# Kernel tuning notes

Hardware: AMD Instinct MI355X
Metric: run time of the kernel (lower is better)

Reference implementation:

```python
import jax, jax.numpy as jnp
import numpy as np

K = 3            # kernel size (odd)
CO, CI = 16, 16  # out/in channels

def setup_inputs() -> dict:
    key = jax.random.key(0)
    k1, k2, k3, k4 = jax.random.split(key, 4)
    B, C, H, W = 4, CI, 128, 128
    input_data = jax.random.normal(k1, (B, C, H, W), dtype=jnp.float32)
    # fixation coordinates in pixel units
    foa_xy = jax.random.uniform(k2, (B, 2), dtype=jnp.float32) * jnp.array([W, H], jnp.float32)
    hidden = 256
    W1 = jax.random.normal(k3, (2, hidden), dtype=jnp.float32) * (1.0 / jnp.sqrt(2.0))
    b1 = jnp.zeros((hidden,), jnp.float32)
    W2 = jax.random.normal(k4, (hidden, CO * CI * K * K), dtype=jnp.float32) * (1.0 / jnp.sqrt(hidden))
    b2 = jnp.zeros((CO * CI * K * K,), jnp.float32)
    return {"input_data": input_data, "foa_xy": foa_xy, "W1": W1, "b1": b1, "W2": W2, "b2": b2}

def _unfold_reflect(x, k):
    # x: [B, C, H, W] -> patches [B, C, k*k, H*W], reflect padding, stride 1, dilation 1
    B, C, H, W = x.shape
    pad = (k - 1) // 2
    xp = jnp.pad(x, ((0, 0), (0, 0), (pad, pad), (pad, pad)), mode="reflect")
    rows = [xp[:, :, i:i + H, j:j + W] for i in range(k) for j in range(k)]
    return jnp.stack(rows, axis=2).reshape(B, C, k * k, H * W)

def reference(input_data, foa_xy, W1, b1, W2, b2):
    B, C, H, W = input_data.shape
    # coordinate grid [H*W, 2] as (x, y), matching torch meshgrid(ij) + stack(xx, yy)
    ys = jnp.arange(H, dtype=jnp.float32)
    xs = jnp.arange(W, dtype=jnp.float32)
    yy, xx = jnp.meshgrid(ys, xs, indexing="ij")
    coords = jnp.stack([xx.ravel(), yy.ravel()], axis=1)         # [HW, 2]
    net_in = (coords[None, :, :] - foa_xy[:, None, :]).reshape(B * H * W, 2)
    # kernel-generating MLP
    h = jax.nn.relu(net_in @ W1 + b1)
    net_out = h @ W2 + b2                                        # [B*HW, CO*CI*K*K]
    kernel = net_out.reshape(B, H * W, CO, CI, K * K)            # [B, P, o, i, q]
    patches = _unfold_reflect(input_data, K)                     # [B, CI, K*K, HW]
    # per-pixel conv: sum over in-channels and kernel taps
    out = jnp.einsum("biqp,bpoiq->bop", patches, kernel)         # [B, CO, HW]
    return out.reshape(B, CO, H, W)
```

## Files before the change

kernel.cpp:

```cpp
#include <hip/hip_runtime.h>

#define CI    16
#define CO    16
#define HID   256
#define KPAD  288
#define NKK   9
#define NCH   144
#define IMGH  128
#define IMGW  128
#define PTS   66
#define KKSTR (NCH * 32)
#define OSTRS (NKK * NCH * 32)

typedef float f32x4  __attribute__((ext_vector_type(4)));
typedef float f32x2  __attribute__((ext_vector_type(2)));
typedef short bf16x8 __attribute__((ext_vector_type(8)));

__device__ __host__ __forceinline__ short f2bf(float f) {
  union { float f; unsigned u; } c; c.f = f;
  unsigned b = c.u + 0x7FFFu + ((c.u >> 16) & 1u);
  return (short)(b >> 16);
}

__global__ void prep_w2(const float* __restrict__ W2, const float* __restrict__ b2,
                        short* __restrict__ W2b) {
  __shared__ float tile[32][65];
  const int kk = blockIdx.x % NKK;
  const int colbase = (blockIdx.x / NKK) * 64;
  const int tid = threadIdx.x;

  for (int e = tid; e < 2048; e += 256) {
    int klr = e >> 6;
    int cc  = e & 63;
    int col = colbase + cc;
    float v;
    if (kk < 8) v = W2[(kk * 32 + klr) * (CO * NCH) + col];
    else        v = (klr == 0) ? b2[col] : 0.f;
    tile[klr][cc] = v;
  }
  __syncthreads();
  for (int e = tid; e < 2048; e += 256) {
    int cc = e >> 5;
    int kl = e & 31;
    int col = colbase + cc;
    int o = col / NCH;
    int n = col - o * NCH;
    W2b[(((o * NKK + kk) * NCH + n) << 5) + kl] = f2bf(tile[kl][cc]);
  }
}

__global__ __launch_bounds__(256, 2)
void ngconv_main(const float* __restrict__ in, const float* __restrict__ foa,
                 const float* __restrict__ W1, const float* __restrict__ b1,
                 const short* __restrict__ W2b, float* __restrict__ out) {
  __shared__ short shHf[36 * 512];
  __shared__ float shPatchT[NCH * PTS];

  const int tid  = threadIdx.x;
  const int lane = tid & 63;
  const int wv   = tid >> 6;
  const int c15  = lane & 15;
  const int quad = lane >> 4;

  const int blk = blockIdx.x;
  const int b   = blk >> 8;
  const int rem = blk & 255;
  const int y   = rem >> 1;
  const int x0  = (rem & 1) << 6;

  const float fx  = foa[b * 2 + 0];
  const float fy  = foa[b * 2 + 1];
  const float dyv = (float)y - fy;

  const int ry0 = (y == 0) ? 1 : (y - 1);
  const int ry2 = (y == IMGH - 1) ? (IMGH - 2) : (y + 1);

  for (int e = tid; e < NCH * 64; e += 256) {
    int n  = e >> 6;
    int px = e & 63;
    int i = n / 9, q = n - i * 9;
    int dyr = q / 3, dx = q - dyr * 3;
    int ryr = (dyr == 0) ? ry0 : ((dyr == 1) ? y : ry2);
    int x = x0 + px + dx - 1;
    x = (x < 0) ? 1 : ((x > IMGW - 1) ? (IMGW - 2) : x);
    shPatchT[n * PTS + px] = in[((b * CI + i) * IMGH + ryr) * IMGW + x];
  }

  for (int g = tid; g < 64 * 36; g += 256) {
    int px = g & 63;
    int ks = g >> 6;
    int k0 = ks << 3;
    float dxv = (float)(x0 + px) - fx;
    short hv[8];
    if (k0 < HID) {
      #pragma unroll
      for (int j = 0; j < 8; ++j) {
        int k = k0 + j;
        float h = fmaxf(fmaf(dxv, W1[k], fmaf(dyv, W1[HID + k], b1[k])), 0.f);
        hv[j] = f2bf(h);
      }
    } else {
      #pragma unroll
      for (int j = 0; j < 8; ++j) hv[j] = (k0 + j == HID) ? f2bf(1.f) : (short)0;
    }
    int ms = px >> 4;
    int kk = k0 >> 5;
    int lslot = ((k0 & 31) >> 3) * 16 + (px & 15);
    *(bf16x8*)&shHf[((ms * NKK + kk) << 9) + (lslot << 3)] = *(bf16x8*)hv;
  }
  __syncthreads();

  #pragma unroll 1
  for (int oj = 0; oj < 4; ++oj) {
    const int o = wv + oj * 4;
    const short* Bo = W2b + o * OSTRS + (c15 << 5) + (quad << 3);

    f32x2 P2[8];
    #pragma unroll
    for (int t = 0; t < 8; ++t) P2[t] = (f32x2){0.f, 0.f};

    #pragma unroll 1
    for (int pass = 0; pass < 3; ++pass) {
      const short* Bp = Bo + (pass * 3) * 512;
      f32x4 acc[4][3];
      #pragma unroll
      for (int ms = 0; ms < 4; ++ms)
        #pragma unroll
        for (int j = 0; j < 3; ++j)
          acc[ms][j] = (f32x4){0.f, 0.f, 0.f, 0.f};

      bf16x8 bE[3], bO[3];
      #pragma unroll
      for (int j = 0; j < 3; ++j) bE[j] = *(const bf16x8*)&Bp[j << 9];

      #pragma unroll 1
      for (int t = 0; t < 4; ++t) {
        const int kkE = 2 * t;
        #pragma unroll
        for (int j = 0; j < 3; ++j)
          bO[j] = *(const bf16x8*)&Bp[(kkE + 1) * KKSTR + (j << 9)];
        {
          const short* hp = shHf + (kkE << 9) + (lane << 3);
          #pragma unroll
          for (int ms = 0; ms < 4; ++ms) {
            bf16x8 af = *(const bf16x8*)&hp[ms * (NKK << 9)];
            #pragma unroll
            for (int j = 0; j < 3; ++j)
              acc[ms][j] = __builtin_amdgcn_mfma_f32_16x16x32_bf16(
                  af, bE[j], acc[ms][j], 0, 0, 0);
          }
        }
        #pragma unroll
        for (int j = 0; j < 3; ++j)
          bE[j] = *(const bf16x8*)&Bp[(kkE + 2) * KKSTR + (j << 9)];
        {
          const short* hp = shHf + ((kkE + 1) << 9) + (lane << 3);
          #pragma unroll
          for (int ms = 0; ms < 4; ++ms) {
            bf16x8 af = *(const bf16x8*)&hp[ms * (NKK << 9)];
            #pragma unroll
            for (int j = 0; j < 3; ++j)
              acc[ms][j] = __builtin_amdgcn_mfma_f32_16x16x32_bf16(
                  af, bO[j], acc[ms][j], 0, 0, 0);
          }
        }
      }
      {
        const short* hp = shHf + (8 << 9) + (lane << 3);
        #pragma unroll
        for (int ms = 0; ms < 4; ++ms) {
          bf16x8 af = *(const bf16x8*)&hp[ms * (NKK << 9)];
          #pragma unroll
          for (int j = 0; j < 3; ++j)
            acc[ms][j] = __builtin_amdgcn_mfma_f32_16x16x32_bf16(
                af, bE[j], acc[ms][j], 0, 0, 0);
        }
      }

      #pragma unroll
      for (int j = 0; j < 3; ++j) {
        int n15 = ((pass * 3 + j) << 4) + c15;
        const float* prow = &shPatchT[n15 * PTS + (quad << 2)];
        #pragma unroll
        for (int ms = 0; ms < 4; ++ms) {
          f32x2 p01 = *(const f32x2*)&prow[ms * 16];
          f32x2 p23 = *(const f32x2*)&prow[ms * 16 + 2];
          f32x2 a01 = {acc[ms][j][0], acc[ms][j][1]};
          f32x2 a23 = {acc[ms][j][2], acc[ms][j][3]};
          P2[ms * 2 + 0] += a01 * p01;
          P2[ms * 2 + 1] += a23 * p23;
        }
      }
    }

    float P[16];
    #pragma unroll
    for (int t = 0; t < 16; ++t) P[t] = P2[t >> 1][t & 1];
    #pragma unroll
    for (int m = 8; m >= 1; m >>= 1) {
      const bool hi = (c15 & m) != 0;
      #pragma unroll
      for (int j = 0; j < m; ++j) {
        float keep = hi ? P[j + m] : P[j];
        float send = hi ? P[j] : P[j + m];
        float recv = __shfl_xor(send, m, 64);
        P[j] = keep + recv;
      }
    }

    const int x = x0 + (c15 >> 2) * 16 + quad * 4 + (c15 & 3);
    out[((b * CO + o) * IMGH + y) * IMGW + x] = P[0];
  }
}

extern "C" void kernel_launch(void* const* d_in, const int* in_sizes, int n_in,
                              void* d_out, int out_size, void* d_ws, size_t ws_size,
                              hipStream_t stream) {
  const float* in  = (const float*)d_in[0];
  const float* foa = (const float*)d_in[1];
  const float* W1  = (const float*)d_in[2];
  const float* b1  = (const float*)d_in[3];
  const float* W2  = (const float*)d_in[4];
  const float* b2  = (const float*)d_in[5];
  float* out = (float*)d_out;
  short* W2b = (short*)d_ws;

  prep_w2<<<324, 256, 0, stream>>>(W2, b2, W2b);
  ngconv_main<<<1024, 256, 0, stream>>>(in, foa, W1, b1, W2b, out);
}
```

Before: 190.0 us.

## Shrink LDS footprint with bf16 patches and register bias fragment to raise occupancy

Patch values are now stored in LDS as bf16 instead of fp32, with the row pitch changed to 68, and unpacked with shifts at use. The bias block of the hidden matrix is no longer kept in LDS; a constant register fragment with a 1.0 in the first element of quad 0 supplies it to the ninth MFMA k-step. Together these cut shared memory per block, and launch bounds now request 3 blocks per CU so more waves can hide latency. The trade-offs are lower precision for the input patches and tighter register limits under the new occupancy target.

Result: faster. 182.9 us (-3.8%).

```diff
diff --git a/kernel.cpp b/kernel.cpp
--- a/kernel.cpp
+++ b/kernel.cpp
@@ -5,10 +5,11 @@
 #define HID   256
 #define KPAD  288
 #define NKK   9
+#define NKH   8
 #define NCH   144
 #define IMGH  128
 #define IMGW  128
-#define PTS   66
+#define PTS   68
 #define KKSTR (NCH * 32)
 #define OSTRS (NKK * NCH * 32)
 
@@ -49,12 +50,12 @@
   }
 }
 
-__global__ __launch_bounds__(256, 2)
+__global__ __launch_bounds__(256, 3)
 void ngconv_main(const float* __restrict__ in, const float* __restrict__ foa,
                  const float* __restrict__ W1, const float* __restrict__ b1,
                  const short* __restrict__ W2b, float* __restrict__ out) {
-  __shared__ short shHf[36 * 512];
-  __shared__ float shPatchT[NCH * PTS];
+  __shared__ short shHf[32 * 512];
+  __shared__ short shPatchT[NCH * PTS];
 
   const int tid  = threadIdx.x;
   const int lane = tid & 63;
@@ -83,31 +84,30 @@
     int ryr = (dyr == 0) ? ry0 : ((dyr == 1) ? y : ry2);
     int x = x0 + px + dx - 1;
     x = (x < 0) ? 1 : ((x > IMGW - 1) ? (IMGW - 2) : x);
-    shPatchT[n * PTS + px] = in[((b * CI + i) * IMGH + ryr) * IMGW + x];
-  }
-
-  for (int g = tid; g < 64 * 36; g += 256) {
+    shPatchT[n * PTS + px] = f2bf(in[((b * CI + i) * IMGH + ryr) * IMGW + x]);
+  }
+
+  for (int g = tid; g < 64 * 32; g += 256) {
     int px = g & 63;
     int ks = g >> 6;
     int k0 = ks << 3;
     float dxv = (float)(x0 + px) - fx;
     short hv[8];
-    if (k0 < HID) {
-      #pragma unroll
-      for (int j = 0; j < 8; ++j) {
-        int k = k0 + j;
-        float h = fmaxf(fmaf(dxv, W1[k], fmaf(dyv, W1[HID + k], b1[k])), 0.f);
-        hv[j] = f2bf(h);
-      }
-    } else {
-      #pragma unroll
-      for (int j = 0; j < 8; ++j) hv[j] = (k0 + j == HID) ? f2bf(1.f) : (short)0;
+    #pragma unroll
+    for (int j = 0; j < 8; ++j) {
+      int k = k0 + j;
+      float h = fmaxf(fmaf(dxv, W1[k], fmaf(dyv, W1[HID + k], b1[k])), 0.f);
+      hv[j] = f2bf(h);
     }
     int ms = px >> 4;
     int kk = k0 >> 5;
     int lslot = ((k0 & 31) >> 3) * 16 + (px & 15);
-    *(bf16x8*)&shHf[((ms * NKK + kk) << 9) + (lslot << 3)] = *(bf16x8*)hv;
-  }
+    *(bf16x8*)&shHf[((ms * NKH + kk) << 9) + (lslot << 3)] = *(bf16x8*)hv;
+  }
+
+  bf16x8 af8 = (bf16x8){0, 0, 0, 0, 0, 0, 0, 0};
+  if (quad == 0) af8[0] = (short)0x3F80;
+
   __syncthreads();
 
   #pragma unroll 1
@@ -143,7 +143,7 @@
           const short* hp = shHf + (kkE << 9) + (lane << 3);
           #pragma unroll
           for (int ms = 0; ms < 4; ++ms) {
-            bf16x8 af = *(const bf16x8*)&hp[ms * (NKK << 9)];
+            bf16x8 af = *(const bf16x8*)&hp[ms * (NKH << 9)];
             #pragma unroll
             for (int j = 0; j < 3; ++j)
               acc[ms][j] = __builtin_amdgcn_mfma_f32_16x16x32_bf16(
@@ -157,7 +157,7 @@
           const short* hp = shHf + ((kkE + 1) << 9) + (lane << 3);
           #pragma unroll
           for (int ms = 0; ms < 4; ++ms) {
-            bf16x8 af = *(const bf16x8*)&hp[ms * (NKK << 9)];
+            bf16x8 af = *(const bf16x8*)&hp[ms * (NKH << 9)];
             #pragma unroll
             for (int j = 0; j < 3; ++j)
               acc[ms][j] = __builtin_amdgcn_mfma_f32_16x16x32_bf16(
@@ -166,29 +166,29 @@
         }
       }
       {
-        const short* hp = shHf + (8 << 9) + (lane << 3);
-        #pragma unroll
-        for (int ms = 0; ms < 4; ++ms) {
-          bf16x8 af = *(const bf16x8*)&hp[ms * (NKK << 9)];
+        #pragma unroll
+        for (int ms = 0; ms < 4; ++ms)
           #pragma unroll
           for (int j = 0; j < 3; ++j)
             acc[ms][j] = __builtin_amdgcn_mfma_f32_16x16x32_bf16(
-                af, bE[j], acc[ms][j], 0, 0, 0);
-        }
+                af8, bE[j], acc[ms][j], 0, 0, 0);
       }
 
       #pragma unroll
       for (int j = 0; j < 3; ++j) {
         int n15 = ((pass * 3 + j) << 4) + c15;
-        const float* prow = &shPatchT[n15 * PTS + (quad << 2)];
+        const short* prow = &shPatchT[n15 * PTS + (quad << 2)];
         #pragma unroll
         for (int ms = 0; ms < 4; ++ms) {
-          f32x2 p01 = *(const f32x2*)&prow[ms * 16];
-          f32x2 p23 = *(const f32x2*)&prow[ms * 16 + 2];
+          uint2 u = *(const uint2*)&prow[ms * 16];
+          float p0 = __uint_as_float(u.x << 16);
+          float p1 = __uint_as_float(u.x & 0xFFFF0000u);
+          float p2 = __uint_as_float(u.y << 16);
+          float p3 = __uint_as_float(u.y & 0xFFFF0000u);
           f32x2 a01 = {acc[ms][j][0], acc[ms][j][1]};
           f32x2 a23 = {acc[ms][j][2], acc[ms][j][3]};
-          P2[ms * 2 + 0] += a01 * p01;
-          P2[ms * 2 + 1] += a23 * p23;
+          P2[ms * 2 + 0] += a01 * (f32x2){p0, p1};
+          P2[ms * 2 + 1] += a23 * (f32x2){p2, p3};
         }
       }
     }
```
